# Performance work log

Measured on AMD Instinct MI355X. Metric: run time of the kernel, lower is better.

## Reference

```python
import jax, jax.numpy as jnp
import numpy as np

B, E, K, HD = 128, 1024, 64, 256


def setup_inputs() -> dict:
    key = jax.random.key(0)
    ks = jax.random.split(key, 9)
    std = 0.01
    ev = jax.random.randint(ks[0], (B, E), 0, K)
    seq = jax.nn.one_hot(ev, K, dtype=jnp.float32)
    lengths = jax.random.randint(ks[1], (B,), E // 2, E + 1)
    mask = jnp.arange(E)[None, :] < lengths[:, None]  # prefix (ragged) mask
    dts = jax.random.uniform(ks[2], (B, E + 1), minval=0.01, maxval=1.0)
    times = jnp.cumsum(dts, axis=1).astype(jnp.float32)  # increasing, [B, E+1]
    U_w = jax.random.normal(ks[3], (7 * HD, K), dtype=jnp.float32) * std
    U_b = jax.random.normal(ks[4], (7 * HD,), dtype=jnp.float32) * std
    V_w = jax.random.normal(ks[5], (7 * HD, HD), dtype=jnp.float32) * std
    V_b = jax.random.normal(ks[6], (7 * HD,), dtype=jnp.float32) * std
    Lw = jax.random.normal(ks[7], (K, HD), dtype=jnp.float32) * std  # L_lamb_til weight
    scale = jnp.ones((K,), dtype=jnp.float32)
    return {"seq": seq, "mask": mask, "times": times, "U_w": U_w, "U_b": U_b,
            "V_w": V_w, "V_b": V_b, "Lw": Lw, "scale": scale}


def reference(seq, mask, times, U_w, U_b, V_w, V_b, Lw, scale):
    Nb, Ne, Kk = seq.shape
    hD = V_w.shape[1]
    sig = jax.nn.sigmoid

    def step(carry, inp):
        ct, cbar, ht = carry
        x, m, tnow, tnext = inp  # [B,K], [B], [B], [B]
        nn = x @ U_w.T + U_b + ht @ V_w.T + V_b  # [B, 7*hD]
        ih, fh, ibh, fbh, zh, oh, dh = jnp.split(nn, 7, axis=1)
        i, f = sig(ih), sig(fh)
        iBar, fBar = sig(ibh), sig(fbh)
        z, o = 2.0 * sig(zh), sig(oh)
        delta = jax.nn.softplus(dh)
        clow = f * ct + i * z
        cbar_new = fBar * cbar + iBar * z
        dt = (tnext - tnow)[:, None]
        ct_new = cbar_new + (clow - cbar_new) * jnp.exp(-dt * delta)
        ht_new = o * (2.0 * sig(2.0 * ct_new) - 1.0)
        lamb_til = ht_new @ Lw.T  # [B, K]
        lamb = scale * jnp.log1p(jnp.exp(lamb_til / scale))
        mm = m[:, None]
        ct2 = jnp.where(mm, ct_new, ct)
        cbar2 = jnp.where(mm, cbar_new, cbar)
        ht2 = jnp.where(mm, ht_new, ht)
        z0 = jnp.zeros((), seq.dtype)
        outs = (jnp.where(mm, lamb, z0), jnp.where(mm, clow, z0),
                jnp.where(mm, cbar_new, z0), jnp.where(mm, delta, z0),
                jnp.where(mm, o, z0))
        return (ct2, cbar2, ht2), outs

    init = (jnp.zeros((Nb, hD), seq.dtype),
            jnp.zeros((Nb, hD), seq.dtype),
            jnp.zeros((Nb, hD), seq.dtype))
    xs = (seq.swapaxes(0, 1), mask.T, times[:, :Ne].T, times[:, 1:Ne + 1].T)
    _, (lambOuts, CLows, Cbars, deltas, OutGates) = jax.lax.scan(step, init, xs)
    # scan stacks along event dim first -> move back to [B, E, *]
    return (lambOuts.swapaxes(0, 1), CLows.swapaxes(0, 1), Cbars.swapaxes(0, 1),
            deltas.swapaxes(0, 1), OutGates.swapaxes(0, 1))
```

## Files before the change

kernel.cpp:

```cpp
#include <hip/hip_runtime.h>
#include <stdint.h>

#define Bn  128
#define En  1024
#define Kn  64
#define HDn 256
#define NGc 8
#define NSc 16

typedef short s8v __attribute__((ext_vector_type(8)));
typedef float f4v __attribute__((ext_vector_type(4)));

static __device__ __forceinline__ unsigned short f2bf(float f) {
  union { float f; unsigned u; } cv; cv.f = f;
  unsigned u = cv.u;
  unsigned r = u + 0x7fffu + ((u >> 16) & 1u);
  return (unsigned short)(r >> 16);
}
static __device__ __forceinline__ float sigm(float x) {
  return 1.0f / (1.0f + __expf(-x));
}

__global__ void detect_mask_fmt(const uint8_t* __restrict__ m8, int* __restrict__ fmt) {
  const int b = blockIdx.x;
  const int e0 = threadIdx.x * 4;
  const uint8_t* row = m8 + (size_t)b * En;
  int bad = 0;
  uint8_t prev = row[e0];
  #pragma unroll
  for (int i = 1; i <= 4; ++i) {
    int e = e0 + i;
    if (e < En) {
      uint8_t cur = row[e];
      if (prev == 0 && cur != 0) bad = 1;
      prev = cur;
    }
  }
  if (threadIdx.x == 0 && row[0] == 0) bad = 1;
  if (bad) atomicOr(fmt, 1);
}

__global__ void compute_ev(const float* __restrict__ seq, int* __restrict__ ev) {
  const int idx  = blockIdx.x * 4 + (threadIdx.x >> 6);
  const int lane = threadIdx.x & 63;
  float v = seq[(size_t)idx * Kn + lane];
  unsigned long long m = __ballot(v > 0.5f);
  if (lane == 0) ev[idx] = __ffsll((long long)m) - 1;
}

__global__ __launch_bounds__(64, 1) void ct_main(
    const float* __restrict__ times, const uint8_t* __restrict__ mask8,
    const float* __restrict__ U_w,  const float* __restrict__ U_b,
    const float* __restrict__ V_w,  const float* __restrict__ V_b,
    const float* __restrict__ Lw,   const float* __restrict__ scale,
    const int* __restrict__ ev,     unsigned short* __restrict__ h_buf,
    int* __restrict__ ctr,          const int* __restrict__ fmtp,
    float* __restrict__ out_lam, float* __restrict__ out_cl,
    float* __restrict__ out_cb,  float* __restrict__ out_dl,
    float* __restrict__ out_og)
{
  __shared__ float U_lds[64 * 16 * 12];

  const int lane = threadIdx.x;
  const int col  = lane & 15;
  const int quad = lane >> 4;
  const int g    = blockIdx.x >> 4;
  const int s    = blockIdx.x & 15;
  const int d0   = s * 16;
  const int fmt  = *fmtp;

  #pragma unroll 1
  for (int i = lane; i < 64 * 16 * 12; i += 64) U_lds[i] = 0.0f;
  #pragma unroll 1
  for (int i = lane; i < 7 * 16 * 64; i += 64) {
    int k = i & 63, dl = (i >> 6) & 15, g7 = i >> 10;
    U_lds[(k * 16 + dl) * 12 + g7] = U_w[(size_t)(g7 * HDn + d0 + dl) * Kn + k];
  }
  __syncthreads();

  s8v Bv[7][8];
  #pragma unroll
  for (int g7 = 0; g7 < 7; ++g7) {
    const float* src = V_w + (size_t)(g7 * HDn + d0 + col) * HDn;
    #pragma unroll
    for (int kc = 0; kc < 8; ++kc) {
      const float* p = src + kc * 32 + quad * 8;
      f4v a = *(const f4v*)(p);
      f4v b = *(const f4v*)(p + 4);
      s8v fr;
      fr[0] = (short)f2bf(a[0]); fr[1] = (short)f2bf(a[1]);
      fr[2] = (short)f2bf(a[2]); fr[3] = (short)f2bf(a[3]);
      fr[4] = (short)f2bf(b[0]); fr[5] = (short)f2bf(b[1]);
      fr[6] = (short)f2bf(b[2]); fr[7] = (short)f2bf(b[3]);
      Bv[g7][kc] = fr;
    }
  }
  s8v BL[8];
  const int kkc = s * 4 + col;
  {
    const bool lv = (col < 4);
    const float* src = Lw + (size_t)(lv ? kkc : 0) * HDn;
    #pragma unroll
    for (int kc = 0; kc < 8; ++kc) {
      const float* p = src + kc * 32 + quad * 8;
      s8v fr;
      #pragma unroll
      for (int j = 0; j < 8; ++j) fr[j] = lv ? (short)f2bf(p[j]) : (short)0;
      BL[kc] = fr;
    }
  }
  float bias[7];
  #pragma unroll
  for (int g7 = 0; g7 < 7; ++g7) {
    int j = g7 * HDn + d0 + col;
    bias[g7] = U_b[j] + V_b[j];
  }
  const float sc = scale[(kkc < Kn) ? kkc : 0];

  float c[4]  = {0, 0, 0, 0}, cb[4] = {0, 0, 0, 0};
  float hreg[4] = {0, 0, 0, 0}, pm[4] = {0, 0, 0, 0};
  int* my_ctr = ctr + g * 32;

  #pragma unroll 1
  for (int t = 0; t <= En; ++t) {
    const bool has_main = (t < En);

    int evv[4]; float dtv[4], mk[4];
    if (has_main) {
      #pragma unroll
      for (int r = 0; r < 4; ++r) {
        const int bglob = g * 16 + quad * 4 + r;
        evv[r] = ev[(size_t)bglob * En + t];
        const float* tp = times + (size_t)bglob * (En + 1) + t;
        dtv[r] = tp[1] - tp[0];
        int mraw;
        if (fmt) mraw = ((const int*)mask8)[(size_t)bglob * En + t];
        else     mraw = (int)mask8[(size_t)bglob * En + t];
        mk[r] = (mraw != 0) ? 1.0f : 0.0f;
      }
    }

    if (t > 0) {
      const int target = NSc * t;
      if (lane == 0) {
        while (__hip_atomic_load(my_ctr, __ATOMIC_ACQUIRE,
                                 __HIP_MEMORY_SCOPE_AGENT) < target) {
          __builtin_amdgcn_s_sleep(1);
        }
      }
    }

    const int par = t & 1;
    const unsigned short* hb = h_buf + (size_t)(par * NGc + g) * 4096;
    s8v A[8];
    #pragma unroll
    for (int kc = 0; kc < 8; ++kc) {
      const int sp = kc * 2 + (quad >> 1);
      A[kc] = *(const s8v*)(hb + sp * 256 + col * 16 + (quad & 1) * 8);
    }

    f4v acc[7] = {}; f4v accL = {0.0f, 0.0f, 0.0f, 0.0f};
    if (has_main) {
      #pragma unroll
      for (int kc = 0; kc < 8; ++kc) {
        accL = __builtin_amdgcn_mfma_f32_16x16x32_bf16(A[kc], BL[kc], accL, 0, 0, 0);
        #pragma unroll
        for (int g7 = 0; g7 < 7; ++g7)
          acc[g7] = __builtin_amdgcn_mfma_f32_16x16x32_bf16(A[kc], Bv[g7][kc], acc[g7], 0, 0, 0);
      }
    } else {
      #pragma unroll
      for (int kc = 0; kc < 8; ++kc)
        accL = __builtin_amdgcn_mfma_f32_16x16x32_bf16(A[kc], BL[kc], accL, 0, 0, 0);
    }

    if (t > 0 && col < 4) {
      #pragma unroll
      for (int r = 0; r < 4; ++r) {
        const int bglob = g * 16 + quad * 4 + r;
        float q   = accL[r] / sc;
        float lam = sc * __logf(1.0f + __expf(q));
        out_lam[((size_t)bglob * En + (t - 1)) * Kn + kkc] =
            (pm[r] != 0.0f) ? lam : 0.0f;
      }
    }

    if (has_main) {
      float clv[4], cbv[4], dlv[4], ogv[4];
      #pragma unroll
      for (int r = 0; r < 4; ++r) {
        const float* up = U_lds + ((size_t)evv[r] * 16 + col) * 12;
        f4v u0 = *(const f4v*)(up);
        f4v u1 = *(const f4v*)(up + 4);
        float nn0 = acc[0][r] + u0[0] + bias[0];
        float nn1 = acc[1][r] + u0[1] + bias[1];
        float nn2 = acc[2][r] + u0[2] + bias[2];
        float nn3 = acc[3][r] + u0[3] + bias[3];
        float nn4 = acc[4][r] + u1[0] + bias[4];
        float nn5 = acc[5][r] + u1[1] + bias[5];
        float nn6 = acc[6][r] + u1[2] + bias[6];
        float i_ = sigm(nn0), f_ = sigm(nn1);
        float ib = sigm(nn2), fb = sigm(nn3);
        float z_ = 2.0f * sigm(nn4), o_ = sigm(nn5);
        float dl = __logf(1.0f + __expf(nn6));
        float clow = f_ * c[r] + i_ * z_;
        float cbn  = fb * cb[r] + ib * z_;
        float ed   = __expf(-dtv[r] * dl);
        float cn   = cbn + (clow - cbn) * ed;
        float hn   = o_ * (2.0f * sigm(2.0f * cn) - 1.0f);
        const bool mb = (mk[r] != 0.0f);
        c[r]    = mb ? cn  : c[r];
        cb[r]   = mb ? cbn : cb[r];
        hreg[r] = mb ? hn  : hreg[r];
        pm[r]   = mk[r];
        clv[r] = mb ? clow : 0.0f;
        cbv[r] = mb ? cbn  : 0.0f;
        dlv[r] = mb ? dl   : 0.0f;
        ogv[r] = mb ? o_   : 0.0f;
      }
      const int par2 = (t + 1) & 1;
      unsigned short* hw =
          h_buf + (size_t)(par2 * NGc + g) * 4096 + (size_t)s * 256;
      #pragma unroll
      for (int r = 0; r < 4; ++r)
        hw[(quad * 4 + r) * 16 + col] = f2bf(hreg[r]);
      if (lane == 0)
        __hip_atomic_fetch_add(my_ctr, 1, __ATOMIC_RELEASE,
                               __HIP_MEMORY_SCOPE_AGENT);
      #pragma unroll
      for (int r = 0; r < 4; ++r) {
        const size_t off =
            ((size_t)(g * 16 + quad * 4 + r) * En + t) * HDn + d0 + col;
        out_cl[off] = clv[r];
        out_cb[off] = cbv[r];
        out_dl[off] = dlv[r];
        out_og[off] = ogv[r];
      }
    }
  }
}

extern "C" void kernel_launch(void* const* d_in, const int* in_sizes, int n_in,
                              void* d_out, int out_size, void* d_ws, size_t ws_size,
                              hipStream_t stream) {
  const float*   seq   = (const float*)d_in[0];
  const uint8_t* mask  = (const uint8_t*)d_in[1];
  const float*   times = (const float*)d_in[2];
  const float*   U_w   = (const float*)d_in[3];
  const float*   U_b   = (const float*)d_in[4];
  const float*   V_w   = (const float*)d_in[5];
  const float*   V_b   = (const float*)d_in[6];
  const float*   Lw    = (const float*)d_in[7];
  const float*   scale = (const float*)d_in[8];

  char* ws = (char*)d_ws;
  unsigned short* h_buf = (unsigned short*)ws;
  int* ctr = (int*)(ws + 131072);
  int* fmt = (int*)(ws + 132096);
  int* ev  = (int*)(ws + 132224);

  hipMemsetAsync(d_ws, 0, 132224, stream);

  detect_mask_fmt<<<dim3(Bn), dim3(256), 0, stream>>>(mask, fmt);
  compute_ev<<<dim3(Bn * En / 4), dim3(256), 0, stream>>>(seq, ev);

  float* out = (float*)d_out;
  float* out_lam = out;
  float* out_cl  = out_lam + (size_t)Bn * En * Kn;
  float* out_cb  = out_cl  + (size_t)Bn * En * HDn;
  float* out_dl  = out_cb  + (size_t)Bn * En * HDn;
  float* out_og  = out_dl  + (size_t)Bn * En * HDn;

  ct_main<<<dim3(NGc * NSc), dim3(64), 0, stream>>>(
      times, mask, U_w, U_b, V_w, V_b, Lw, scale,
      ev, h_buf, ctr, fmt, out_lam, out_cl, out_cb, out_dl, out_og);
}
```

Before: 6.625 ms.

## Relax inter-block sync, pack h stores, reorder critical path of recurrent step

Replaces acquire/release atomics on the per-group step counter with relaxed atomics, relaxed atomic loads and stores of the h buffer, and an explicit vmcnt wait, so each handoff avoids cache-invalidating fences. Packs two bf16 h values per 32-bit store via a lane shuffle, hoists the U table lookups before the spin-wait, and moves the lambda MFMA and its output after the h publish so the critical path is shorter. Output stores become nontemporal. Relying on relaxed ordering plus s_waitcnt for cross-block visibility is subtle and could be fragile.

```diff
diff --git a/kernel.cpp b/kernel.cpp
--- a/kernel.cpp
+++ b/kernel.cpp
@@ -117,6 +117,8 @@
   }
   const float sc = scale[(kkc < Kn) ? kkc : 0];
 
+  unsigned int* hbuf32 = (unsigned int*)h_buf;
+
   float c[4]  = {0, 0, 0, 0}, cb[4] = {0, 0, 0, 0};
   float hreg[4] = {0, 0, 0, 0}, pm[4] = {0, 0, 0, 0};
   int* my_ctr = ctr + g * 32;
@@ -126,6 +128,7 @@
     const bool has_main = (t < En);
 
     int evv[4]; float dtv[4], mk[4];
+    f4v u0v[4], u1v[4];
     if (has_main) {
       #pragma unroll
       for (int r = 0; r < 4; ++r) {
@@ -138,67 +141,68 @@
         else     mraw = (int)mask8[(size_t)bglob * En + t];
         mk[r] = (mraw != 0) ? 1.0f : 0.0f;
       }
-    }
+      #pragma unroll
+      for (int r = 0; r < 4; ++r) {
+        const float* up = U_lds + ((size_t)evv[r] * 16 + col) * 12;
+        u0v[r] = *(const f4v*)(up);
+        u1v[r] = *(const f4v*)(up + 4);
+      }
+    }
+
+    float pmo[4];
+    #pragma unroll
+    for (int r = 0; r < 4; ++r) pmo[r] = pm[r];
 
     if (t > 0) {
       const int target = NSc * t;
       if (lane == 0) {
-        while (__hip_atomic_load(my_ctr, __ATOMIC_ACQUIRE,
+        while (__hip_atomic_load(my_ctr, __ATOMIC_RELAXED,
                                  __HIP_MEMORY_SCOPE_AGENT) < target) {
           __builtin_amdgcn_s_sleep(1);
         }
       }
+      __builtin_amdgcn_sched_barrier(0);
+      asm volatile("" ::: "memory");
     }
 
     const int par = t & 1;
-    const unsigned short* hb = h_buf + (size_t)(par * NGc + g) * 4096;
+    const unsigned int* hb32 = hbuf32 + (size_t)(par * NGc + g) * 2048;
     s8v A[8];
     #pragma unroll
     for (int kc = 0; kc < 8; ++kc) {
-      const int sp = kc * 2 + (quad >> 1);
-      A[kc] = *(const s8v*)(hb + sp * 256 + col * 16 + (quad & 1) * 8);
+      const int base = (kc * 2 + (quad >> 1)) * 128 + col * 8 + (quad & 1) * 4;
+      union { unsigned int u[4]; s8v v; } cvt;
+      #pragma unroll
+      for (int j = 0; j < 4; ++j)
+        cvt.u[j] = __hip_atomic_load(hb32 + base + j, __ATOMIC_RELAXED,
+                                     __HIP_MEMORY_SCOPE_AGENT);
+      A[kc] = cvt.v;
     }
 
     f4v acc[7] = {}; f4v accL = {0.0f, 0.0f, 0.0f, 0.0f};
     if (has_main) {
       #pragma unroll
       for (int kc = 0; kc < 8; ++kc) {
-        accL = __builtin_amdgcn_mfma_f32_16x16x32_bf16(A[kc], BL[kc], accL, 0, 0, 0);
         #pragma unroll
         for (int g7 = 0; g7 < 7; ++g7)
           acc[g7] = __builtin_amdgcn_mfma_f32_16x16x32_bf16(A[kc], Bv[g7][kc], acc[g7], 0, 0, 0);
       }
-    } else {
-      #pragma unroll
-      for (int kc = 0; kc < 8; ++kc)
-        accL = __builtin_amdgcn_mfma_f32_16x16x32_bf16(A[kc], BL[kc], accL, 0, 0, 0);
-    }
-
-    if (t > 0 && col < 4) {
-      #pragma unroll
-      for (int r = 0; r < 4; ++r) {
-        const int bglob = g * 16 + quad * 4 + r;
-        float q   = accL[r] / sc;
-        float lam = sc * __logf(1.0f + __expf(q));
-        out_lam[((size_t)bglob * En + (t - 1)) * Kn + kkc] =
-            (pm[r] != 0.0f) ? lam : 0.0f;
-      }
-    }
-
+    }
+    #pragma unroll
+    for (int kc = 0; kc < 8; ++kc)
+      accL = __builtin_amdgcn_mfma_f32_16x16x32_bf16(A[kc], BL[kc], accL, 0, 0, 0);
+
+    float clv[4], cbv[4], dlv[4], ogv[4];
     if (has_main) {
-      float clv[4], cbv[4], dlv[4], ogv[4];
-      #pragma unroll
-      for (int r = 0; r < 4; ++r) {
-        const float* up = U_lds + ((size_t)evv[r] * 16 + col) * 12;
-        f4v u0 = *(const f4v*)(up);
-        f4v u1 = *(const f4v*)(up + 4);
-        float nn0 = acc[0][r] + u0[0] + bias[0];
-        float nn1 = acc[1][r] + u0[1] + bias[1];
-        float nn2 = acc[2][r] + u0[2] + bias[2];
-        float nn3 = acc[3][r] + u0[3] + bias[3];
-        float nn4 = acc[4][r] + u1[0] + bias[4];
-        float nn5 = acc[5][r] + u1[1] + bias[5];
-        float nn6 = acc[6][r] + u1[2] + bias[6];
+      #pragma unroll
+      for (int r = 0; r < 4; ++r) {
+        float nn0 = acc[0][r] + u0v[r][0] + bias[0];
+        float nn1 = acc[1][r] + u0v[r][1] + bias[1];
+        float nn2 = acc[2][r] + u0v[r][2] + bias[2];
+        float nn3 = acc[3][r] + u0v[r][3] + bias[3];
+        float nn4 = acc[4][r] + u1v[r][0] + bias[4];
+        float nn5 = acc[5][r] + u1v[r][1] + bias[5];
+        float nn6 = acc[6][r] + u1v[r][2] + bias[6];
         float i_ = sigm(nn0), f_ = sigm(nn1);
         float ib = sigm(nn2), fb = sigm(nn3);
         float z_ = 2.0f * sigm(nn4), o_ = sigm(nn5);
@@ -218,23 +222,53 @@
         dlv[r] = mb ? dl   : 0.0f;
         ogv[r] = mb ? o_   : 0.0f;
       }
+
       const int par2 = (t + 1) & 1;
-      unsigned short* hw =
-          h_buf + (size_t)(par2 * NGc + g) * 4096 + (size_t)s * 256;
-      #pragma unroll
-      for (int r = 0; r < 4; ++r)
-        hw[(quad * 4 + r) * 16 + col] = f2bf(hreg[r]);
+      unsigned int* hw32 = hbuf32 + (size_t)(par2 * NGc + g) * 2048 + s * 128;
+      float hsw[4];
+      #pragma unroll
+      for (int r = 0; r < 4; ++r) hsw[r] = __shfl_xor(hreg[r], 1, 64);
+      const int evn = (col & 1);
+      unsigned int w[4];
+      #pragma unroll
+      for (int r = 0; r < 4; ++r) {
+        unsigned int a  = f2bf(hreg[r]);
+        unsigned int bn = f2bf(hsw[r]);
+        w[r] = evn ? (bn | (a << 16)) : (a | (bn << 16));
+      }
+      const unsigned int wa = evn ? w[2] : w[0];
+      const unsigned int wb = evn ? w[3] : w[1];
+      const int ra = evn ? 2 : 0;
+      __hip_atomic_store(hw32 + (quad * 4 + ra) * 8 + (col >> 1), wa,
+                         __ATOMIC_RELAXED, __HIP_MEMORY_SCOPE_AGENT);
+      __hip_atomic_store(hw32 + (quad * 4 + ra + 1) * 8 + (col >> 1), wb,
+                         __ATOMIC_RELAXED, __HIP_MEMORY_SCOPE_AGENT);
+      asm volatile("s_waitcnt vmcnt(0)" ::: "memory");
       if (lane == 0)
-        __hip_atomic_fetch_add(my_ctr, 1, __ATOMIC_RELEASE,
+        __hip_atomic_fetch_add(my_ctr, 1, __ATOMIC_RELAXED,
                                __HIP_MEMORY_SCOPE_AGENT);
+    }
+
+    if (t > 0 && col < 4) {
+      #pragma unroll
+      for (int r = 0; r < 4; ++r) {
+        const int bglob = g * 16 + quad * 4 + r;
+        float q   = accL[r] / sc;
+        float lam = sc * __logf(1.0f + __expf(q));
+        __builtin_nontemporal_store((pmo[r] != 0.0f) ? lam : 0.0f,
+            &out_lam[((size_t)bglob * En + (t - 1)) * Kn + kkc]);
+      }
+    }
+
+    if (has_main) {
       #pragma unroll
       for (int r = 0; r < 4; ++r) {
         const size_t off =
             ((size_t)(g * 16 + quad * 4 + r) * En + t) * HDn + d0 + col;
-        out_cl[off] = clv[r];
-        out_cb[off] = cbv[r];
-        out_dl[off] = dlv[r];
-        out_og[off] = ogv[r];
+        __builtin_nontemporal_store(clv[r], &out_cl[off]);
+        __builtin_nontemporal_store(cbv[r], &out_cb[off]);
+        __builtin_nontemporal_store(dlv[r], &out_dl[off]);
+        __builtin_nontemporal_store(ogv[r], &out_og[off]);
       }
     }
   }
```

Result: faster. 5.553 ms (-16.2%).
